# Kernel tuning notes

Measured on AMD Instinct MI355X. Metric: run time of the kernel, lower is better.

## Reference

```python
import jax, jax.numpy as jnp
import numpy as np

B, T, C = 2, 2048, 2048
N_HEADS = 16
D_HEAD = C // N_HEADS


def setup_inputs() -> dict:
    key = jax.random.key(0)
    k1, k2, k3 = jax.random.split(key, 3)
    x = jax.random.normal(k1, (B, T, C), dtype=jnp.float32)
    # torch Linear weights stored as [out,in]; we store transposed [in,out] for x @ W
    Wqkv = jax.random.normal(k2, (C, 3 * C), dtype=jnp.float32) * (C ** -0.5)
    Wout = jax.random.normal(k3, (C, C), dtype=jnp.float32) * (C ** -0.5)
    # causal mask: scores where mask==0 are set to -inf
    mask = jnp.tril(jnp.ones((T, T), dtype=bool))[None, None]  # [1,1,T,T]
    return {"x": x, "mask": mask, "Wqkv": Wqkv, "Wout": Wout}


def reference(x, mask, Wqkv, Wout):
    Bx, Tx, Cx = x.shape
    qkv = x @ Wqkv                                   # [B,T,3C]
    q, k, v = jnp.split(qkv, 3, axis=-1)

    def split_heads(t):
        return t.reshape(Bx, Tx, N_HEADS, D_HEAD).transpose(0, 2, 1, 3)  # [B,H,T,Dh]

    q, k, v = split_heads(q), split_heads(k), split_heads(v)
    scale = D_HEAD ** -0.5
    scores = jnp.einsum('bhqd,bhkd->bhqk', q, k) * scale   # [B,H,T,T]
    scores = jnp.where(mask, scores, -jnp.inf)
    attn = jax.nn.softmax(scores, axis=-1)
    # dropout p=0.0 -> identity
    out = jnp.einsum('bhqk,bhkd->bhqd', attn, v)           # [B,H,T,Dh]
    out = out.transpose(0, 2, 1, 3).reshape(Bx, Tx, Cx)
    return out @ Wout
```

## Files before the change

### kernel.cpp

```cpp
#include <hip/hip_runtime.h>
#include <stdint.h>

typedef __bf16 bf16x8 __attribute__((ext_vector_type(8)));
typedef float f32x4 __attribute__((ext_vector_type(4)));
typedef unsigned short u16x8 __attribute__((ext_vector_type(8)));
typedef unsigned int u32x4 __attribute__((ext_vector_type(4)));

__device__ __forceinline__ unsigned short f2bf(float f) {
    unsigned int u = __builtin_bit_cast(unsigned int, f);
    unsigned int r = u + 0x7fffu + ((u >> 16) & 1u);
    return (unsigned short)(r >> 16);
}

__device__ __forceinline__ unsigned int cvt_pk_bf16(float a, float b) {
    unsigned int r;
    asm("v_cvt_pk_bf16_f32 %0, %1, %2" : "=v"(r) : "v"(a), "v"(b));
    return r;
}

__device__ __forceinline__ void async16(const void* g, void* l) {
    __builtin_amdgcn_global_load_lds(
        (const __attribute__((address_space(1))) void*)g,
        (__attribute__((address_space(3))) void*)l, 16, 0, 0);
}

__global__ __launch_bounds__(256) void cast_bf16(
    const float* __restrict__ src, unsigned short* __restrict__ dst, int n8)
{
    int i = blockIdx.x * 256 + threadIdx.x;
    if (i >= n8) return;
    const float* f = src + (size_t)i * 8;
    f32x4 a = *reinterpret_cast<const f32x4*>(f);
    f32x4 b = *reinterpret_cast<const f32x4*>(f + 4);
    u16x8 r;
    r[0]=f2bf(a[0]); r[1]=f2bf(a[1]); r[2]=f2bf(a[2]); r[3]=f2bf(a[3]);
    r[4]=f2bf(b[0]); r[5]=f2bf(b[1]); r[6]=f2bf(b[2]); r[7]=f2bf(b[3]);
    *reinterpret_cast<u16x8*>(dst + (size_t)i * 8) = r;
}

__global__ __launch_bounds__(256) void transpose_cast_f32(
    const float* __restrict__ src, unsigned short* __restrict__ dst, int R, int Cc)
{
    __shared__ unsigned short St[64 * 64];
    const int tid = threadIdx.x;
    const int r0 = blockIdx.y * 64, c0 = blockIdx.x * 64;
    const int lr  = tid >> 2;
    const int lcb = (tid & 3) * 16;
    const float* sp = src + (size_t)(r0 + lr) * Cc + c0 + lcb;
    #pragma unroll
    for (int u = 0; u < 4; u++) {
        f32x4 v = *reinterpret_cast<const f32x4*>(sp + 4 * u);
        #pragma unroll
        for (int e = 0; e < 4; e++) {
            int c = lcb + 4 * u + e;
            St[c * 64 + (((lr >> 3) ^ ((c >> 4) & 3)) << 3) + (lr & 7)] = f2bf(v[e]);
        }
    }
    __syncthreads();
    #pragma unroll
    for (int i = 0; i < 2; i++) {
        int ck = tid + 256 * i;
        int c = ck >> 3, ch = ck & 7;
        u16x8 val = *reinterpret_cast<const u16x8*>(&St[c * 64 + ((ch ^ ((c >> 4) & 3)) << 3)]);
        *reinterpret_cast<u16x8*>(dst + (size_t)(c0 + c) * R + r0 + ch * 8) = val;
    }
}

__global__ __launch_bounds__(256) void vtrans(
    const unsigned short* __restrict__ qkv, unsigned short* __restrict__ VT)
{
    const int T = 2048, CH = 6144;
    __shared__ unsigned short St[64 * 64];
    const int tid = threadIdx.x;
    const int bh = blockIdx.z;
    const int b = bh >> 4, h = bh & 15;
    const int t0 = blockIdx.x * 64, d0 = blockIdx.y * 64;
    const int lr  = tid >> 2;
    const int lcb = (tid & 3) * 16;
    const unsigned short* sp = qkv + (size_t)(b * T + t0 + lr) * CH + 4096 + h * 128 + d0 + lcb;
    u16x8 v0 = *reinterpret_cast<const u16x8*>(sp);
    u16x8 v1 = *reinterpret_cast<const u16x8*>(sp + 8);
    #pragma unroll
    for (int e = 0; e < 8; e++) {
        int c = lcb + e;
        St[c * 64 + (((lr >> 3) ^ ((c >> 4) & 3)) << 3) + (lr & 7)] = v0[e];
        c = lcb + 8 + e;
        St[c * 64 + (((lr >> 3) ^ ((c >> 4) & 3)) << 3) + (lr & 7)] = v1[e];
    }
    __syncthreads();
    #pragma unroll
    for (int i = 0; i < 2; i++) {
        int ck = tid + 256 * i;
        int d = ck >> 3, ch = ck & 7;
        const int Q = ch & 3, B32 = ch >> 2;
        u16x8 val;
        #pragma unroll
        for (int e = 0; e < 4; e++) {
            int ta = 32 * B32 + 4 * Q + e;
            int tb = ta + 16;
            val[e]     = St[d * 64 + (((ta >> 3) ^ ((d >> 4) & 3)) << 3) + (ta & 7)];
            val[4 + e] = St[d * 64 + (((tb >> 3) ^ ((d >> 4) & 3)) << 3) + (tb & 7)];
        }
        *reinterpret_cast<u16x8*>(VT + (size_t)(bh * 128 + d0 + d) * T + t0 + ch * 8) = val;
    }
}

__global__ __launch_bounds__(256) void gemm_bt(
    const unsigned short* __restrict__ A,
    const unsigned short* __restrict__ BT,
    void* __restrict__ C, int M, int N, int K, int cF32)
{
    __shared__ unsigned short As[128 * 32];
    __shared__ unsigned short Bs[128 * 32];
    const int tid = threadIdx.x;
    const int w = tid >> 6, lane = tid & 63;
    const int quad = lane >> 4, l16 = lane & 15;
    const int wm = (w >> 1) * 64, wn = (w & 1) * 64;
    const int m0 = blockIdx.y * 128, n0 = blockIdx.x * 128;

    const int srow = w * 16 + (lane >> 2);
    const int scol = (lane & 3) * 8;
    const unsigned short* aG = A  + (size_t)(m0 + srow) * K + scol;
    const unsigned short* bG = BT + (size_t)(n0 + srow) * K + scol;
    unsigned short* aL = As + (w * 16) * 32;
    unsigned short* bL = Bs + (w * 16) * 32;

    f32x4 acc[4][4] = {};

    for (int k0 = 0; k0 < K; k0 += 32) {
        async16(aG + k0, aL);
        async16(aG + (size_t)64 * K + k0, aL + 64 * 32);
        async16(bG + k0, bL);
        async16(bG + (size_t)64 * K + k0, bL + 64 * 32);
        __syncthreads();

        bf16x8 af[4], bf[4];
        #pragma unroll
        for (int i = 0; i < 4; i++)
            af[i] = *reinterpret_cast<const bf16x8*>(&As[(wm + i * 16 + l16) * 32 + quad * 8]);
        #pragma unroll
        for (int c = 0; c < 4; c++)
            bf[c] = *reinterpret_cast<const bf16x8*>(&Bs[(wn + c * 16 + l16) * 32 + quad * 8]);
        #pragma unroll
        for (int i = 0; i < 4; i++)
            #pragma unroll
            for (int c = 0; c < 4; c++)
                acc[i][c] = __builtin_amdgcn_mfma_f32_16x16x32_bf16(af[i], bf[c], acc[i][c], 0, 0, 0);
        __syncthreads();
    }

    #pragma unroll
    for (int i = 0; i < 4; i++)
        #pragma unroll
        for (int c = 0; c < 4; c++)
            #pragma unroll
            for (int r = 0; r < 4; r++) {
                const int row = m0 + wm + i * 16 + quad * 4 + r;
                const int col = n0 + wn + c * 16 + l16;
                const size_t off = (size_t)row * N + col;
                if (cF32) ((float*)C)[off] = acc[i][c][r];
                else ((unsigned short*)C)[off] = f2bf(acc[i][c][r]);
            }
}

__global__ __launch_bounds__(256, 2) void flash_attn(
    const unsigned short* __restrict__ qkv,
    const unsigned short* __restrict__ VT,
    unsigned short* __restrict__ Out)
{
    const int T = 2048, CH = 6144;
    __shared__ unsigned short KsBuf[2][64 * 128];
    __shared__ unsigned short VtBuf[2][128 * 64];

    const int tid = threadIdx.x;
    const int w = tid >> 6, lane = tid & 63;
    const int quad = lane >> 4, l16 = lane & 15;
    const int bh = blockIdx.y, b = bh >> 4, h = bh & 15;
    const int q0 = (gridDim.x - 1 - blockIdx.x) * 128;

    const float sc = 0.08838834764831845f * 1.4426950408889634f;
    const float NINF = -__builtin_inff();

    bf16x8 qf[2][4];
    #pragma unroll
    for (int st = 0; st < 2; st++) {
        const unsigned short* qrow = qkv + (size_t)(b * T + q0 + w * 32 + st * 16 + l16) * CH + h * 128;
        #pragma unroll
        for (int dc = 0; dc < 4; dc++) {
            u16x8 raw = *reinterpret_cast<const u16x8*>(qrow + dc * 32 + quad * 8);
            u16x8 scl;
            #pragma unroll
            for (int e = 0; e < 8; e++) {
                float f = __builtin_bit_cast(float, (unsigned int)raw[e] << 16);
                scl[e] = f2bf(f * sc);
            }
            qf[st][dc] = __builtin_bit_cast(bf16x8, scl);
        }
    }

    f32x4 o[2][8] = {};
    float m_i[2] = {NINF, NINF};
    float l_i[2] = {0.f, 0.f};
    const int xsw = l16 & 7;

    const int kRow = (lane >> 4);
    const int kCh  = lane & 15;
    const int vRow = (lane >> 3);
    const int vCh  = lane & 7;

    auto stageKV = [&](int kv0, unsigned short* kp, unsigned short* vp) {
        #pragma unroll
        for (int i = 0; i < 4; i++) {
            const int r0 = i * 16 + w * 4;
            const int kv = r0 + kRow;
            const int ch = kCh ^ (kv & 7);
            async16(qkv + (size_t)(b * T + kv0 + kv) * CH + 2048 + h * 128 + ch * 8,
                    kp + r0 * 128);
        }
        #pragma unroll
        for (int i = 0; i < 4; i++) {
            const int r0 = i * 32 + w * 8;
            const int d = r0 + vRow;
            const int ch = vCh ^ (d & 7);
            async16(VT + ((size_t)bh * 128 + d) * T + kv0 + ch * 8,
                    vp + r0 * 64);
        }
    };

    unsigned short* kc = KsBuf[0];
    unsigned short* vc = VtBuf[0];
    unsigned short* kn = KsBuf[1];
    unsigned short* vn = VtBuf[1];

    const int nt = (q0 + 128) / 64;

    stageKV(0, kc, vc);
    asm volatile("s_waitcnt vmcnt(0)\n\ts_barrier" ::: "memory");

    for (int t = 0; t < nt; ++t) {
        const int kv0 = t * 64;
        if (t + 1 < nt) stageKV((t + 1) * 64, kn, vn);

        f32x4 s[2][4] = {};
        __builtin_amdgcn_s_setprio(1);
        #pragma unroll
        for (int dc = 0; dc < 4; dc++)
            #pragma unroll
            for (int ntt = 0; ntt < 4; ntt++) {
                bf16x8 kf = *reinterpret_cast<const bf16x8*>(
                    &kc[(ntt * 16 + l16) * 128 + (((dc * 4 + quad) ^ xsw) << 3)]);
                s[0][ntt] = __builtin_amdgcn_mfma_f32_16x16x32_bf16(kf, qf[0][dc], s[0][ntt], 0, 0, 0);
                s[1][ntt] = __builtin_amdgcn_mfma_f32_16x16x32_bf16(kf, qf[1][dc], s[1][ntt], 0, 0, 0);
            }
        __builtin_amdgcn_s_setprio(0);

        unsigned int pk[2][4][2];
        #pragma unroll
        for (int st = 0; st < 2; st++) {
            const int qs = q0 + w * 32 + st * 16;
            const int qrow = qs + l16;
            if (kv0 + 63 > qs) {
                #pragma unroll
                for (int ntt = 0; ntt < 4; ntt++)
                    #pragma unroll
                    for (int r = 0; r < 4; r++)
                        if (kv0 + ntt * 16 + quad * 4 + r > qrow) s[st][ntt][r] = NINF;
            }
            float mx = fmaxf(fmaxf(fmaxf(s[st][0][0], s[st][0][1]), fmaxf(s[st][0][2], s[st][0][3])),
                             fmaxf(fmaxf(s[st][1][0], s[st][1][1]), fmaxf(s[st][1][2], s[st][1][3])));
            mx = fmaxf(mx,
                 fmaxf(fmaxf(fmaxf(s[st][2][0], s[st][2][1]), fmaxf(s[st][2][2], s[st][2][3])),
                       fmaxf(fmaxf(s[st][3][0], s[st][3][1]), fmaxf(s[st][3][2], s[st][3][3]))));
            mx = fmaxf(mx, __shfl_xor(mx, 16));
            mx = fmaxf(mx, __shfl_xor(mx, 32));

            const float mold = m_i[st];
            if (!__all(mx <= mold + 8.0f)) {
                const float mnew = fmaxf(mold, mx);
                const float alpha = exp2f(mold - mnew);
                m_i[st] = mnew;
                l_i[st] *= alpha;
                #pragma unroll
                for (int r = 0; r < 4; r++) {
                    const float a = __shfl(alpha, quad * 4 + r);
                    #pragma unroll
                    for (int c = 0; c < 8; c++) o[st][c][r] *= a;
                }
            }
            const float m = m_i[st];
            float p[4][4];
            #pragma unroll
            for (int ntt = 0; ntt < 4; ntt++)
                #pragma unroll
                for (int r = 0; r < 4; r++)
                    p[ntt][r] = exp2f(s[st][ntt][r] - m);
            float ps = ((p[0][0] + p[0][1]) + (p[0][2] + p[0][3]))
                     + ((p[1][0] + p[1][1]) + (p[1][2] + p[1][3]))
                     + ((p[2][0] + p[2][1]) + (p[2][2] + p[2][3]))
                     + ((p[3][0] + p[3][1]) + (p[3][2] + p[3][3]));
            ps += __shfl_xor(ps, 16);
            ps += __shfl_xor(ps, 32);
            l_i[st] += ps;
            #pragma unroll
            for (int ntt = 0; ntt < 4; ntt++) {
                pk[st][ntt][0] = cvt_pk_bf16(p[ntt][0], p[ntt][1]);
                pk[st][ntt][1] = cvt_pk_bf16(p[ntt][2], p[ntt][3]);
            }
        }

        __builtin_amdgcn_s_setprio(1);
        #pragma unroll
        for (int kc2 = 0; kc2 < 2; kc2++) {
            u32x4 a0, a1;
            a0[0] = pk[0][2*kc2][0];   a0[1] = pk[0][2*kc2][1];
            a0[2] = pk[0][2*kc2+1][0]; a0[3] = pk[0][2*kc2+1][1];
            a1[0] = pk[1][2*kc2][0];   a1[1] = pk[1][2*kc2][1];
            a1[2] = pk[1][2*kc2+1][0]; a1[3] = pk[1][2*kc2+1][1];
            const bf16x8 pf0 = __builtin_bit_cast(bf16x8, a0);
            const bf16x8 pf1 = __builtin_bit_cast(bf16x8, a1);
            #pragma unroll
            for (int c = 0; c < 8; c++) {
                bf16x8 vf = *reinterpret_cast<const bf16x8*>(
                    &vc[(c * 16 + l16) * 64 + (((kc2 * 4 + quad) ^ xsw) << 3)]);
                o[0][c] = __builtin_amdgcn_mfma_f32_16x16x32_bf16(pf0, vf, o[0][c], 0, 0, 0);
                o[1][c] = __builtin_amdgcn_mfma_f32_16x16x32_bf16(pf1, vf, o[1][c], 0, 0, 0);
            }
        }
        __builtin_amdgcn_s_setprio(0);

        asm volatile("s_waitcnt vmcnt(0) lgkmcnt(0)\n\ts_barrier" ::: "memory");

        unsigned short* tp;
        tp = kc; kc = kn; kn = tp;
        tp = vc; vc = vn; vn = tp;
    }

    #pragma unroll
    for (int st = 0; st < 2; st++)
        #pragma unroll
        for (int r = 0; r < 4; r++) {
            const float linv = 1.0f / __shfl(l_i[st], quad * 4 + r);
            const int row = q0 + w * 32 + st * 16 + quad * 4 + r;
            const size_t base = (size_t)(b * T + row) * 2048 + h * 128;
            #pragma unroll
            for (int c = 0; c < 8; c++)
                Out[base + c * 16 + l16] = f2bf(o[st][c][r] * linv);
        }
}

extern "C" void kernel_launch(void* const* d_in, const int* in_sizes, int n_in,
                              void* d_out, int out_size, void* d_ws, size_t ws_size,
                              hipStream_t stream) {
    const int B = 2, T = 2048, C = 2048;
    const float* x    = (const float*)d_in[0];
    const float* Wqkv = (const float*)d_in[2];
    const float* Wout = (const float*)d_in[3];
    const int M = B * T;

    char* ws = (char*)d_ws;
    unsigned short* qkv   = (unsigned short*)ws;
    unsigned short* xb    = (unsigned short*)(ws + 50331648);
    unsigned short* WoutT = xb;
    unsigned short* WqkvT = (unsigned short*)(ws + 67108864);
    unsigned short* VTp   = WqkvT;
    unsigned short* O     = (unsigned short*)(ws + 92274688);

    cast_bf16<<<dim3(M * C / 8 / 256), 256, 0, stream>>>(x, xb, M * C / 8);
    transpose_cast_f32<<<dim3(3 * C / 64, C / 64), 256, 0, stream>>>(Wqkv, WqkvT, C, 3 * C);
    gemm_bt<<<dim3(3 * C / 128, M / 128), 256, 0, stream>>>(xb, WqkvT, qkv, M, 3 * C, C, 0);
    vtrans<<<dim3(T / 64, 2, B * 16), 256, 0, stream>>>(qkv, VTp);
    transpose_cast_f32<<<dim3(C / 64, C / 64), 256, 0, stream>>>(Wout, WoutT, C, C);
    flash_attn<<<dim3(T / 128, B * 16), 256, 0, stream>>>(qkv, VTp, O);
    gemm_bt<<<dim3(C / 128, M / 128), 256, 0, stream>>>(O, WoutT, d_out, M, C, C, 1);
}
```

Before: 451.8 us.

## Double-buffer LDS tiles in bf16 GEMM to overlap global loads with MFMA

The GEMM kernel now keeps two LDS buffers for the A and B tiles. It issues async global-to-LDS loads for the next K tile before running the MFMAs on the current one, and uses one waitcnt plus barrier per iteration instead of two syncthreads. It also raises wave priority around the MFMA block. This is meant to hide global load latency behind compute, at the cost of twice the LDS per block and therefore possible occupancy pressure.

Result: faster. 421.6 us (-6.7%).

```diff
diff --git a/kernel.cpp b/kernel.cpp
--- a/kernel.cpp
+++ b/kernel.cpp
@@ -110,8 +110,8 @@
     const unsigned short* __restrict__ BT,
     void* __restrict__ C, int M, int N, int K, int cF32)
 {
-    __shared__ unsigned short As[128 * 32];
-    __shared__ unsigned short Bs[128 * 32];
+    __shared__ unsigned short As[2][128 * 32];
+    __shared__ unsigned short Bs[2][128 * 32];
     const int tid = threadIdx.x;
     const int w = tid >> 6, lane = tid & 63;
     const int quad = lane >> 4, l16 = lane & 15;
@@ -122,31 +122,45 @@
     const int scol = (lane & 3) * 8;
     const unsigned short* aG = A  + (size_t)(m0 + srow) * K + scol;
     const unsigned short* bG = BT + (size_t)(n0 + srow) * K + scol;
-    unsigned short* aL = As + (w * 16) * 32;
-    unsigned short* bL = Bs + (w * 16) * 32;
+    const int ldsO = (w * 16) * 32;
 
     f32x4 acc[4][4] = {};
-
-    for (int k0 = 0; k0 < K; k0 += 32) {
-        async16(aG + k0, aL);
-        async16(aG + (size_t)64 * K + k0, aL + 64 * 32);
-        async16(bG + k0, bL);
-        async16(bG + (size_t)64 * K + k0, bL + 64 * 32);
-        __syncthreads();
+    const int nkt = K >> 5;
+
+    async16(aG, &As[0][ldsO]);
+    async16(aG + (size_t)64 * K, &As[0][ldsO + 64 * 32]);
+    async16(bG, &Bs[0][ldsO]);
+    async16(bG + (size_t)64 * K, &Bs[0][ldsO + 64 * 32]);
+    asm volatile("s_waitcnt vmcnt(0)\n\ts_barrier" ::: "memory");
+
+    int ct = 0;
+    for (int t = 0; t < nkt; ++t) {
+        if (t + 1 < nkt) {
+            const int k1 = (t + 1) * 32;
+            async16(aG + k1, &As[ct ^ 1][ldsO]);
+            async16(aG + (size_t)64 * K + k1, &As[ct ^ 1][ldsO + 64 * 32]);
+            async16(bG + k1, &Bs[ct ^ 1][ldsO]);
+            async16(bG + (size_t)64 * K + k1, &Bs[ct ^ 1][ldsO + 64 * 32]);
+        }
 
         bf16x8 af[4], bf[4];
         #pragma unroll
         for (int i = 0; i < 4; i++)
-            af[i] = *reinterpret_cast<const bf16x8*>(&As[(wm + i * 16 + l16) * 32 + quad * 8]);
+            af[i] = *reinterpret_cast<const bf16x8*>(&As[ct][(wm + i * 16 + l16) * 32 + quad * 8]);
         #pragma unroll
         for (int c = 0; c < 4; c++)
-            bf[c] = *reinterpret_cast<const bf16x8*>(&Bs[(wn + c * 16 + l16) * 32 + quad * 8]);
+            bf[c] = *reinterpret_cast<const bf16x8*>(&Bs[ct][(wn + c * 16 + l16) * 32 + quad * 8]);
+
+        __builtin_amdgcn_s_setprio(1);
         #pragma unroll
         for (int i = 0; i < 4; i++)
             #pragma unroll
             for (int c = 0; c < 4; c++)
                 acc[i][c] = __builtin_amdgcn_mfma_f32_16x16x32_bf16(af[i], bf[c], acc[i][c], 0, 0, 0);
-        __syncthreads();
+        __builtin_amdgcn_s_setprio(0);
+
+        asm volatile("s_waitcnt vmcnt(0) lgkmcnt(0)\n\ts_barrier" ::: "memory");
+        ct ^= 1;
     }
 
     #pragma unroll
```
